# Performance work log

Hardware: AMD Instinct MI355X
Metric: run time of the kernel (lower is better)

The kernel has to match this reference:

```python
import jax, jax.numpy as jnp
import numpy as np

N_NODES = 50000      # nodes
N_EDGES = 800000     # directed edges (avg degree 16)
HIDDEN = 128
F_IN = 11            # QM9 num_node_features
NUM_CLASSES = 19     # QM9 num targets
NUM_GRAPHS = 2048


def _glorot(key, fan_in, fan_out):
    lim = np.sqrt(6.0 / (fan_in + fan_out)).astype(np.float32)
    return jax.random.uniform(key, (fan_in, fan_out), jnp.float32, -lim, lim)


def setup_inputs() -> dict:
    key = jax.random.key(0)
    ks = jax.random.split(key, 8)
    x = jax.random.normal(ks[0], (N_NODES, F_IN), jnp.float32)
    edge_index = jax.random.randint(ks[1], (2, N_EDGES), 0, N_NODES, dtype=jnp.int64)
    batch = jnp.sort(jax.random.randint(ks[2], (N_NODES,), 0, NUM_GRAPHS, dtype=jnp.int64))
    W1 = _glorot(ks[3], F_IN, HIDDEN); b1 = jnp.zeros((HIDDEN,), jnp.float32)
    W2 = _glorot(ks[4], HIDDEN, HIDDEN); b2 = jnp.zeros((HIDDEN,), jnp.float32)
    W3 = _glorot(ks[5], HIDDEN, HIDDEN); b3 = jnp.zeros((HIDDEN,), jnp.float32)
    Wl = _glorot(ks[6], HIDDEN, NUM_CLASSES); bl = jnp.zeros((NUM_CLASSES,), jnp.float32)
    return dict(x=x, edge_index=edge_index, batch=batch,
                W1=W1, b1=b1, W2=W2, b2=b2, W3=W3, b3=b3, Wl=Wl, bl=bl)


def gcn_conv(x, src, dst, W, b, n):
    """PyG GCNConv: x' = D^-1/2 (A + I) D^-1/2 (x W) + b, degrees include self-loops."""
    h = x @ W                                                      # [n, out]
    deg = jax.ops.segment_sum(jnp.ones_like(dst, h.dtype), dst, num_segments=n) + 1.0
    dinv = jax.lax.rsqrt(deg)                                      # [n]
    norm = dinv[src] * dinv[dst]                                   # [E]
    agg = jax.ops.segment_sum(h[src] * norm[:, None], dst, num_segments=n)
    agg = agg + h * (dinv * dinv)[:, None]                         # self-loop term
    return agg + b


def reference(x, edge_index, batch, W1, b1, W2, b2, W3, b3, Wl, bl):
    src, dst = edge_index[0], edge_index[1]
    h = jax.nn.relu(gcn_conv(x, src, dst, W1, b1, N_NODES))
    h = jax.nn.relu(gcn_conv(h, src, dst, W2, b2, N_NODES))
    h = gcn_conv(h, src, dst, W3, b3, N_NODES)
    # global_mean_pool over graph ids
    sums = jax.ops.segment_sum(h, batch, num_segments=NUM_GRAPHS)
    cnt = jax.ops.segment_sum(jnp.ones((N_NODES,), h.dtype), batch, num_segments=NUM_GRAPHS)
    pooled = sums / jnp.maximum(cnt, 1.0)[:, None]                 # [G, H]
    # dropout is identity in eval mode
    return pooled @ Wl + bl                                        # [G, NUM_CLASSES]
```

## Files before the change

### kernel.cpp

```cpp
#include <hip/hip_runtime.h>
#include <hip/hip_bf16.h>
#include <hip/hip_fp16.h>


#define HIDDEN 128
#define F_IN 11
#define NCLS 19
#define NBITS 9
#define NB 128
#define RNODES 512
#define EPB 8192
#define OUTL_CAP 10240

typedef _Float16 half8 __attribute__((ext_vector_type(8)));
typedef float floatx4 __attribute__((ext_vector_type(4)));


__global__ void scatter_kernel(const int* __restrict__ src, const int* __restrict__ dst,
                               int* __restrict__ bcur, unsigned int* __restrict__ bents,
                               int E, int cap) {
    __shared__ int hist[NB];
    __shared__ int binoff[NB];
    __shared__ int runrel[NB];
    __shared__ unsigned int ebuf[EPB];
    __shared__ unsigned short binOf[EPB];
    __shared__ int cw[2];
    int tid = threadIdx.x, lane = tid & 63, w = tid >> 6;
    int base = blockIdx.x * EPB;
    int cnt = min(EPB, E - base);
    for (int i = tid; i < NB; i += 256) hist[i] = 0;
    __syncthreads();
    unsigned int pk[32];
    int rk[32];
#pragma unroll
    for (int j = 0; j < 32; ++j) {
        int idx = tid + 256 * j;
        if (idx < cnt) {
            int e = base + idx;
            int s = src[e], d = dst[e];
            pk[j] = (unsigned int)s | ((unsigned int)d << 16);
            int bin = d >> NBITS;
            int r = atomicAdd(&hist[bin], 1);
            rk[j] = r | (bin << 16);
        } else rk[j] = -1;
    }
    __syncthreads();
    int v = 0, xv = 0;
    if (tid < NB) {
        v = hist[tid]; xv = v;
#pragma unroll
        for (int d = 1; d < 64; d <<= 1) {
            int t = __shfl_up(xv, d, 64);
            if (lane >= d) xv += t;
        }
        if (lane == 63) cw[w] = xv;
    }
    __syncthreads();
    if (tid < NB) {
        binoff[tid] = xv - v + ((w == 1) ? cw[0] : 0);
        runrel[tid] = v ? atomicAdd(&bcur[tid], v) : 0;
    }
    __syncthreads();
#pragma unroll
    for (int j = 0; j < 32; ++j) {
        if (rk[j] >= 0) {
            int bin = rk[j] >> 16, r = rk[j] & 0xFFFF;
            int pos = binoff[bin] + r;
            ebuf[pos] = pk[j];
            binOf[pos] = (unsigned short)bin;
        }
    }
    __syncthreads();
    for (int i = tid; i < cnt; i += 256) {
        int bin = binOf[i];
        int rel = runrel[bin] + (i - binoff[bin]);
        if (rel < cap)
            bents[bin * cap + rel] = ebuf[i];
    }
}

__global__ void build_kernel(const unsigned int* __restrict__ bents, const int* __restrict__ bcur,
                             const float* __restrict__ x, const int* __restrict__ batch,
                             int2* __restrict__ begend, unsigned short* __restrict__ csr16,
                             float* __restrict__ dinv, float* __restrict__ gcnt,
                             __half* __restrict__ x16h, int n, int cap, int rst) {
    __shared__ int counts[RNODES];
    __shared__ int lcur[RNODES];
    __shared__ unsigned short outl[OUTL_CAP];
    __shared__ int wsums[8];
    int tid = threadIdx.x;
    int lane = tid & 63, w = tid >> 6;
    int b = blockIdx.x;
    int base = b << NBITS;
    int nn = min(RNODES, n - base);
    int ebase = b * cap;
    int ecnt = min(bcur[b], cap);
    int st = b * rst;
    for (int i = tid; i < RNODES; i += 1024) counts[i] = 0;
    __syncthreads();
    for (int e = tid; e < ecnt; e += 1024)
        atomicAdd(&counts[(bents[ebase + e] >> 16) - base], 1);
    __syncthreads();
    int v = 0, xv = 0;
    if (tid < RNODES) {
        v = (tid < nn) ? counts[tid] + 1 : 0;
        xv = v;
#pragma unroll
        for (int d = 1; d < 64; d <<= 1) {
            int t = __shfl_up(xv, d, 64);
            if (lane >= d) xv += t;
        }
        if (lane == 63) wsums[w] = xv;
    }
    __syncthreads();
    if (tid < 64) {
        int s = (lane < 8) ? wsums[lane] : 0;
#pragma unroll
        for (int d = 1; d < 8; d <<= 1) {
            int t = __shfl_up(s, d, 64);
            if (lane >= d) s += t;
        }
        if (lane < 8) wsums[lane] = s;
    }
    __syncthreads();
    if (tid < nn) {
        int excl = xv - v + ((w > 0) ? wsums[w - 1] : 0);
        lcur[tid] = excl + 1;
        outl[excl] = (unsigned short)(base + tid);
        begend[base + tid] = make_int2(st + excl, st + excl + v);
        atomicAdd(&gcnt[batch[base + tid]], 1.0f);
    }
    __syncthreads();
    for (int e = tid; e < ecnt; e += 1024) {
        unsigned int pk = bents[ebase + e];
        int i = (int)(pk >> 16) - base;
        int r = atomicAdd(&lcur[i], 1);
        outl[r] = (unsigned short)(pk & 0xFFFFu);
    }
    __syncthreads();
    int total = ecnt + nn;
    for (int i = tid; i < total; i += 1024)
        csr16[st + i] = outl[i];
    for (int idx = tid; idx < nn * 16; idx += 1024) {
        int i = idx >> 4, j = idx & 15;
        float di = 1.0f / sqrtf((float)(counts[i] + 1));
        if (j == 0) dinv[base + i] = di;
        float xv2 = (j < F_IN) ? x[(long)(base + i) * F_IN + j] * di : 0.f;
        x16h[(long)(base + i) * 16 + j] = __float2half(xv2);
    }
}


__global__ void agg16_gemm_kernel(const __half* __restrict__ x16h, const int2* __restrict__ begend,
                                  const unsigned short* __restrict__ csr16,
                                  const float* __restrict__ dinv, const float* __restrict__ W1,
                                  const float* __restrict__ b1, __half* __restrict__ h1h, int n) {
    __shared__ float2 W1s[F_IN][64];
    __shared__ float2 bs[64];
    int tid = threadIdx.x;
    for (int i = tid; i < F_IN * 64; i += 256) {
        int k = i >> 6, j = i & 63;
        W1s[k][j] = make_float2(W1[k * HIDDEN + 2 * j], W1[k * HIDDEN + 2 * j + 1]);
    }
    if (tid < 64) bs[tid] = make_float2(b1[2 * tid], b1[2 * tid + 1]);
    __syncthreads();
    int node = (int)(((long)blockIdx.x * blockDim.x + threadIdx.x) >> 6);
    int lane = threadIdx.x & 63;
    if (node >= n) return;
    int grp = lane >> 4, f = lane & 15;
    int2 be = begend[node];
    int beg = be.x, end = be.y;
    float acc = 0.f;
    int eb = beg;
    for (; eb + 16 <= end; eb += 16) {
        int s[4]; __half v[4];
#pragma unroll
        for (int j = 0; j < 4; ++j) s[j] = csr16[eb + grp + 4 * j];
#pragma unroll
        for (int j = 0; j < 4; ++j) v[j] = x16h[(long)s[j] * 16 + f];
#pragma unroll
        for (int j = 0; j < 4; ++j) acc += __half2float(v[j]);
    }
    if (eb + 8 <= end) {
        int s0 = csr16[eb + grp], s1 = csr16[eb + grp + 4];
        acc += __half2float(x16h[(long)s0 * 16 + f]) + __half2float(x16h[(long)s1 * 16 + f]);
        eb += 8;
    }
    for (int e = eb + grp; e < end; e += 4)
        acc += __half2float(x16h[(long)csr16[e] * 16 + f]);
    acc += __shfl_down(acc, 32);
    acc += __shfl_down(acc, 16);
    float z = acc * dinv[node];
    float2 o = bs[lane];
#pragma unroll
    for (int k = 0; k < F_IN; ++k) {
        float zk = __shfl(z, k);
        float2 w = W1s[k][lane];
        o.x += zk * w.x;
        o.y += zk * w.y;
    }
    __half2 h = __floats2half2_rn(fmaxf(o.x, 0.f), fmaxf(o.y, 0.f));
    ((__half2*)h1h)[(long)node * 64 + lane] = h;
}


__global__ __launch_bounds__(256) void gemm_mfma_kernel(
        const __half* __restrict__ h1h, const float* __restrict__ W2,
        const float* __restrict__ dinv, __half* __restrict__ hsh, int n) {
    __shared__ _Float16 W2T[128 * 136];
    __shared__ _Float16 outs[64 * 136];
    int tid = threadIdx.x;
    for (int i = tid; i < 128 * 128; i += 256) {
        int k = i >> 7, nn = i & 127;
        W2T[nn * 136 + k] = (_Float16)W2[i];
    }
    int base = blockIdx.x * 64;
    int lane = tid & 63, wid = tid >> 6;
    int l15 = lane & 15, quad = lane >> 4;
    int arow = base + wid * 16 + l15;
    if (arow >= n) arow = n - 1;
    const _Float16* Aptr = (const _Float16*)h1h + (size_t)arow * 128;
    floatx4 acc[8];
#pragma unroll
    for (int t = 0; t < 8; ++t) acc[t] = (floatx4){0.f, 0.f, 0.f, 0.f};
    __syncthreads();
#pragma unroll
    for (int c = 0; c < 4; ++c) {
        half8 a = *(const half8*)(Aptr + c * 32 + quad * 8);
#pragma unroll
        for (int t = 0; t < 8; ++t) {
            half8 b = *(const half8*)(&W2T[(t * 16 + l15) * 136 + c * 32 + quad * 8]);
            acc[t] = __builtin_amdgcn_mfma_f32_16x16x32_f16(a, b, acc[t], 0, 0, 0);
        }
    }
    float dv[4];
#pragma unroll
    for (int r = 0; r < 4; ++r) {
        int nd = base + wid * 16 + quad * 4 + r;
        dv[r] = dinv[(nd < n) ? nd : 0];
    }
#pragma unroll
    for (int t = 0; t < 8; ++t)
#pragma unroll
        for (int r = 0; r < 4; ++r)
            outs[(wid * 16 + quad * 4 + r) * 136 + t * 16 + l15] = (_Float16)(acc[t][r] * dv[r]);
    __syncthreads();
    for (int i = tid; i < 64 * 16; i += 256) {
        int ln = i >> 4, qq = i & 15;
        long nd = base + ln;
        if (nd < n) {
            uint4 u = *(uint4*)&outs[ln * 136 + qq * 8];
            ((uint4*)hsh)[nd * 16 + qq] = u;
        }
    }
}


__global__ void agg128h_kernel(const __half* __restrict__ hsh, const int2* __restrict__ begend,
                               const unsigned short* __restrict__ csr16, const float* __restrict__ dinv,
                               const float* __restrict__ bias, __half* __restrict__ outh, int n) {
    int node = (int)(((long)blockIdx.x * blockDim.x + threadIdx.x) >> 6);
    int lane = threadIdx.x & 63;
    if (node >= n) return;
    int grp = lane >> 5, q = lane & 31;
    int2 be = begend[node];
    int beg = be.x, end = be.y;
    float4 acc = make_float4(0.f, 0.f, 0.f, 0.f);
    int eb = beg;
    for (; eb + 16 <= end; eb += 16) {
        int s[8]; uint2 u[8];
#pragma unroll
        for (int j = 0; j < 8; ++j) s[j] = csr16[eb + grp + 2 * j];
#pragma unroll
        for (int j = 0; j < 8; ++j) u[j] = ((const uint2*)hsh)[(long)s[j] * 32 + q];
#pragma unroll
        for (int j = 0; j < 8; ++j) {
            float2 lo = __half22float2(*(__half2*)&u[j].x);
            float2 hi = __half22float2(*(__half2*)&u[j].y);
            acc.x += lo.x; acc.y += lo.y; acc.z += hi.x; acc.w += hi.y;
        }
    }
    if (eb + 8 <= end) {
        int s[4]; uint2 u[4];
#pragma unroll
        for (int j = 0; j < 4; ++j) s[j] = csr16[eb + grp + 2 * j];
#pragma unroll
        for (int j = 0; j < 4; ++j) u[j] = ((const uint2*)hsh)[(long)s[j] * 32 + q];
#pragma unroll
        for (int j = 0; j < 4; ++j) {
            float2 lo = __half22float2(*(__half2*)&u[j].x);
            float2 hi = __half22float2(*(__half2*)&u[j].y);
            acc.x += lo.x; acc.y += lo.y; acc.z += hi.x; acc.w += hi.y;
        }
        eb += 8;
    }
    for (int e = eb + grp; e < end; e += 2) {
        uint2 u = ((const uint2*)hsh)[(long)csr16[e] * 32 + q];
        float2 lo = __half22float2(*(__half2*)&u.x);
        float2 hi = __half22float2(*(__half2*)&u.y);
        acc.x += lo.x; acc.y += lo.y; acc.z += hi.x; acc.w += hi.y;
    }
    acc.x += __shfl_down(acc.x, 32);
    acc.y += __shfl_down(acc.y, 32);
    acc.z += __shfl_down(acc.z, 32);
    acc.w += __shfl_down(acc.w, 32);
    if (grp == 0) {
        float di = dinv[node];
        float4 b = ((const float4*)bias)[q];
        __half2 h01 = __floats2half2_rn(fmaxf(acc.x * di + b.x, 0.f), fmaxf(acc.y * di + b.y, 0.f));
        __half2 h23 = __floats2half2_rn(fmaxf(acc.z * di + b.z, 0.f), fmaxf(acc.w * di + b.w, 0.f));
        uint2 u = make_uint2(*(unsigned int*)&h01, *(unsigned int*)&h23);
        ((uint2*)outh)[(long)node * 32 + q] = u;
    }
}


__global__ void w3l_kernel(const float* __restrict__ W3, const float* __restrict__ Wl,
                           const float* __restrict__ b3, float* __restrict__ W3l,
                           float* __restrict__ b3l) {
    __shared__ float Wls[HIDDEN * NCLS];
    int tid = threadIdx.x;
    for (int i = tid; i < HIDDEN * NCLS; i += 256) Wls[i] = Wl[i];
    __syncthreads();
    if (blockIdx.x < 10) {
        int o = blockIdx.x * 256 + tid;
        if (o < HIDDEN * NCLS) {
            int i = o / NCLS, j = o % NCLS;
            float acc = 0.f;
#pragma unroll 8
            for (int k = 0; k < HIDDEN; ++k) acc += W3[i * HIDDEN + k] * Wls[k * NCLS + j];
            W3l[o] = acc;
        }
    } else if (tid < NCLS) {
        float acc = 0.f;
#pragma unroll 8
        for (int k = 0; k < HIDDEN; ++k) acc += b3[k] * Wls[k * NCLS + tid];
        b3l[tid] = acc;
    }
}

__global__ void gemm_y32h_kernel(const __half* __restrict__ h2h, const float* __restrict__ W3l,
                                 const float* __restrict__ dinv, __half* __restrict__ ys, int n) {
    __shared__ float hs[12][HIDDEN];
    __shared__ float Ws[HIDDEN][20];
    int tid = threadIdx.x;
    long base = (long)blockIdx.x * 12;
    for (int i = tid; i < HIDDEN * NCLS; i += 256) Ws[i / NCLS][i % NCLS] = W3l[i];
    for (int idx = tid; idx < 12 * 32; idx += 256) {
        int node = idx >> 5, q = idx & 31;
        long gn = base + node;
        uint2 u = (gn < n) ? ((const uint2*)h2h)[gn * 32 + q] : make_uint2(0u, 0u);
        float2 lo = __half22float2(*(__half2*)&u.x);
        float2 hi = __half22float2(*(__half2*)&u.y);
        hs[node][q * 4] = lo.x; hs[node][q * 4 + 1] = lo.y;
        hs[node][q * 4 + 2] = hi.x; hs[node][q * 4 + 3] = hi.y;
    }
    __syncthreads();
    if (tid < 12 * NCLS) {
        int node = tid / NCLS, j = tid % NCLS;
        long gn = base + node;
        if (gn < n) {
            float acc = 0.f;
#pragma unroll 8
            for (int k = 0; k < HIDDEN; ++k) acc += hs[node][k] * Ws[k][j];
            ys[gn * 32 + j] = __float2half(acc * dinv[gn]);
        }
    }
    for (int idx = tid; idx < 12 * 13; idx += 256) {
        int node = idx / 13, j = 19 + idx % 13;
        long gn = base + node;
        if (gn < n) ys[gn * 32 + j] = __half(0.f);
    }
}

__global__ void agg24h_pool_kernel(const __half* __restrict__ ys, const int2* __restrict__ begend,
                                   const unsigned short* __restrict__ csr16, const float* __restrict__ dinv,
                                   const int* __restrict__ batch, float* __restrict__ pool, int n) {
    int node = (int)(((long)blockIdx.x * blockDim.x + threadIdx.x) >> 6);
    int lane = threadIdx.x & 63;
    if (node >= n) return;
    int grp = lane >> 4, f = lane & 15;
    int2 be = begend[node];
    int beg = be.x, end = be.y;
    float2 acc = {0.f, 0.f};
    int eb = beg;
    for (; eb + 32 <= end; eb += 32) {
        int s[8]; unsigned int u[8];
#pragma unroll
        for (int j = 0; j < 8; ++j) s[j] = csr16[eb + grp + 4 * j];
#pragma unroll
        for (int j = 0; j < 8; ++j) u[j] = ((const unsigned int*)ys)[(long)s[j] * 16 + f];
#pragma unroll
        for (int j = 0; j < 8; ++j) {
            float2 v = __half22float2(*(__half2*)&u[j]);
            acc.x += v.x; acc.y += v.y;
        }
    }
    if (eb + 16 <= end) {
        int s[4]; unsigned int u[4];
#pragma unroll
        for (int j = 0; j < 4; ++j) s[j] = csr16[eb + grp + 4 * j];
#pragma unroll
        for (int j = 0; j < 4; ++j) u[j] = ((const unsigned int*)ys)[(long)s[j] * 16 + f];
#pragma unroll
        for (int j = 0; j < 4; ++j) {
            float2 v = __half22float2(*(__half2*)&u[j]);
            acc.x += v.x; acc.y += v.y;
        }
        eb += 16;
    }
    for (int e = eb + grp; e < end; e += 4) {
        unsigned int u = ((const unsigned int*)ys)[(long)csr16[e] * 16 + f];
        float2 v = __half22float2(*(__half2*)&u);
        acc.x += v.x; acc.y += v.y;
    }
    acc.x += __shfl_down(acc.x, 32);
    acc.y += __shfl_down(acc.y, 32);
    acc.x += __shfl_down(acc.x, 16);
    acc.y += __shfl_down(acc.y, 16);
    if (lane < 16) {
        int g = batch[node];
        float sc = dinv[node];
        int c0 = 2 * f;
        if (c0 < NCLS) atomicAdd(&pool[(long)g * 24 + c0], acc.x * sc);
        if (c0 + 1 < NCLS) atomicAdd(&pool[(long)g * 24 + c0 + 1], acc.y * sc);
    }
}

__global__ void final_kernel(const float* __restrict__ pool, const float* __restrict__ cnt,
                             const float* __restrict__ b3l, const float* __restrict__ bl,
                             float* __restrict__ out, int G) {
    int i = blockIdx.x * blockDim.x + threadIdx.x;
    if (i >= G * NCLS) return;
    int g = i / NCLS, j = i % NCLS;
    float c = cnt[g];
    out[i] = (c > 0.f) ? pool[(long)g * 24 + j] / c + b3l[j] + bl[j] : bl[j];
}


static inline size_t align256(size_t x) { return (x + 255) & ~(size_t)255; }

extern "C" void kernel_launch(void* const* d_in, const int* in_sizes, int n_in,
                              void* d_out, int out_size, void* d_ws, size_t ws_size,
                              hipStream_t stream) {
    const float* x    = (const float*)d_in[0];
    const int*   ei   = (const int*)d_in[1];
    const int*   batch= (const int*)d_in[2];
    const float* W1   = (const float*)d_in[3];
    const float* b1   = (const float*)d_in[4];
    const float* W2   = (const float*)d_in[5];
    const float* b2   = (const float*)d_in[6];
    const float* W3   = (const float*)d_in[7];
    const float* b3   = (const float*)d_in[8];
    const float* Wl   = (const float*)d_in[9];
    const float* bl   = (const float*)d_in[10];
    float* out = (float*)d_out;

    const int N = in_sizes[0] / F_IN;
    const int E = in_sizes[1] / 2;
    const int G = out_size / NCLS;
    const int* src = ei;
    const int* dst = ei + E;
    const int nSB = (E + EPB - 1) / EPB;
    const int nBK = (N + RNODES - 1) / RNODES;
    int cap = (int)((long long)E * RNODES / N) + 1024;
    if (cap + RNODES > OUTL_CAP) cap = OUTL_CAP - RNODES;
    const int rst = cap + RNODES;

    char* p = (char*)d_ws;
    size_t off = 0;
    unsigned int*   bents  = (unsigned int*)(p + off);   off = align256(off + (size_t)NB * cap * 4);
    unsigned short* csr16  = (unsigned short*)(p + off); off = align256(off + (size_t)NB * rst * 2);
    int2*           begend = (int2*)(p + off);           off = align256(off + (size_t)N * 8);
    float*          dinv   = (float*)(p + off);          off = align256(off + (size_t)N * 4);
    __half*         x16h   = (__half*)(p + off);         off = align256(off + (size_t)N * 16 * 2);
    __half*         h1h    = (__half*)(p + off);         off = align256(off + (size_t)N * HIDDEN * 2);
    __half*         hsh    = (__half*)(p + off);         off = align256(off + (size_t)N * HIDDEN * 2);
    __half*         h2h    = (__half*)(p + off);         off = align256(off + (size_t)N * HIDDEN * 2);
    __half*         y32h   = (__half*)(p + off);         off = align256(off + (size_t)N * 32 * 2);
    float*          W3l    = (float*)(p + off);          off = align256(off + (size_t)HIDDEN * NCLS * 4);
    float*          b3l    = (float*)(p + off);          off = align256(off + (size_t)NCLS * 4);
    float*          pool   = (float*)(p + off);
    float*          gcnt   = pool + (size_t)G * 24;
    int*            bcur   = (int*)(pool + (size_t)G * 25);
    off = align256(off + (size_t)G * 25 * 4 + NB * 4);
    (void)ws_size; (void)n_in;

    hipMemsetAsync(pool, 0, (size_t)G * 25 * 4 + NB * 4, stream);

    scatter_kernel<<<nSB, 256, 0, stream>>>(src, dst, bcur, bents, E, cap);
    build_kernel<<<nBK, 1024, 0, stream>>>(bents, bcur, x, batch, begend, csr16,
                                           dinv, gcnt, x16h, N, cap, rst);
    w3l_kernel<<<11, 256, 0, stream>>>(W3, Wl, b3, W3l, b3l);

    const int aggBlocks = (N + 3) / 4;

    agg16_gemm_kernel<<<aggBlocks, 256, 0, stream>>>(x16h, begend, csr16, dinv, W1, b1, h1h, N);

    gemm_mfma_kernel<<<(N + 63) / 64, 256, 0, stream>>>(h1h, W2, dinv, hsh, N);
    agg128h_kernel<<<aggBlocks, 256, 0, stream>>>(hsh, begend, csr16, dinv, b2, h2h, N);

    gemm_y32h_kernel<<<(N + 11) / 12, 256, 0, stream>>>(h2h, W3l, dinv, y32h, N);
    agg24h_pool_kernel<<<aggBlocks, 256, 0, stream>>>(y32h, begend, csr16, dinv, batch, pool, N);
    final_kernel<<<(G * NCLS + 255) / 256, 256, 0, stream>>>(pool, gcnt, b3l, bl, out, G);
}
```

Before: 247.2 us.

## Shrink CSR bucket size, fold weight prep into scatter kernel, pretranspose W2

Halves the node-bucket width (256 nodes per bucket, 256 buckets) and edges per scatter block, so the build kernel runs with 512 threads and uses less shared memory. This gives more blocks and better occupancy in the CSR construction. The separate W3·Wl kernel is removed and its work, plus a one-time fp16 transpose of W2, runs in extra blocks of the scatter launch. The MFMA GEMM then copies the transposed W2 with vector loads instead of converting fp32 element by element in every block. The smaller bucket capacity margin raises overflow risk for skewed degree distributions.

Measured after the change: 231.0 us, median of 2. 1.07x faster.

```diff
diff --git a/kernel.cpp b/kernel.cpp
--- a/kernel.cpp
+++ b/kernel.cpp
@@ -6,11 +6,11 @@
 #define HIDDEN 128
 #define F_IN 11
 #define NCLS 19
-#define NBITS 9
-#define NB 128
-#define RNODES 512
-#define EPB 8192
-#define OUTL_CAP 10240
+#define NBITS 8
+#define NB 256
+#define RNODES 256
+#define EPB 4096
+#define OUTL_CAP 5376
 
 typedef _Float16 half8 __attribute__((ext_vector_type(8)));
 typedef float floatx4 __attribute__((ext_vector_type(4)));
@@ -18,22 +18,60 @@
 
 __global__ void scatter_kernel(const int* __restrict__ src, const int* __restrict__ dst,
                                int* __restrict__ bcur, unsigned int* __restrict__ bents,
-                               int E, int cap) {
+                               int E, int cap, int nSB,
+                               const float* __restrict__ W3, const float* __restrict__ Wl,
+                               const float* __restrict__ b3, float* __restrict__ W3l,
+                               float* __restrict__ b3l, const float* __restrict__ W2,
+                               __half* __restrict__ W2Th) {
     __shared__ int hist[NB];
     __shared__ int binoff[NB];
     __shared__ int runrel[NB];
     __shared__ unsigned int ebuf[EPB];
     __shared__ unsigned short binOf[EPB];
-    __shared__ int cw[2];
+    __shared__ int cw[4];
     int tid = threadIdx.x, lane = tid & 63, w = tid >> 6;
+
+    if (blockIdx.x >= nSB) {
+        int xb = blockIdx.x - nSB;
+        if (xb < 11) {
+            float* Wls = (float*)ebuf;
+            for (int i = tid; i < HIDDEN * NCLS; i += 256) Wls[i] = Wl[i];
+            __syncthreads();
+            if (xb < 10) {
+                int o = xb * 256 + tid;
+                if (o < HIDDEN * NCLS) {
+                    int i = o / NCLS, j = o % NCLS;
+                    float acc = 0.f;
+#pragma unroll 8
+                    for (int k = 0; k < HIDDEN; ++k) acc += W3[i * HIDDEN + k] * Wls[k * NCLS + j];
+                    W3l[o] = acc;
+                }
+            } else if (tid < NCLS) {
+                float acc = 0.f;
+#pragma unroll 8
+                for (int k = 0; k < HIDDEN; ++k) acc += b3[k] * Wls[k * NCLS + tid];
+                b3l[tid] = acc;
+            }
+        } else {
+            int base = (xb - 11) * 4096;
+#pragma unroll
+            for (int r = 0; r < 16; ++r) {
+                int idx = base + tid + 256 * r;
+                int k = idx >> 7, nn2 = idx & 127;
+                W2Th[nn2 * HIDDEN + k] = __float2half(W2[idx]);
+            }
+        }
+        return;
+    }
+
     int base = blockIdx.x * EPB;
     int cnt = min(EPB, E - base);
     for (int i = tid; i < NB; i += 256) hist[i] = 0;
     __syncthreads();
-    unsigned int pk[32];
-    int rk[32];
-#pragma unroll
-    for (int j = 0; j < 32; ++j) {
+    unsigned int pk[16];
+    int rk[16];
+#pragma unroll
+    for (int j = 0; j < 16; ++j) {
         int idx = tid + 256 * j;
         if (idx < cnt) {
             int e = base + idx;
@@ -45,24 +83,21 @@
         } else rk[j] = -1;
     }
     __syncthreads();
-    int v = 0, xv = 0;
-    if (tid < NB) {
-        v = hist[tid]; xv = v;
-#pragma unroll
-        for (int d = 1; d < 64; d <<= 1) {
-            int t = __shfl_up(xv, d, 64);
-            if (lane >= d) xv += t;
-        }
-        if (lane == 63) cw[w] = xv;
-    }
-    __syncthreads();
-    if (tid < NB) {
-        binoff[tid] = xv - v + ((w == 1) ? cw[0] : 0);
-        runrel[tid] = v ? atomicAdd(&bcur[tid], v) : 0;
-    }
-    __syncthreads();
-#pragma unroll
-    for (int j = 0; j < 32; ++j) {
+    int v = hist[tid], xv = v;
+#pragma unroll
+    for (int d = 1; d < 64; d <<= 1) {
+        int t = __shfl_up(xv, d, 64);
+        if (lane >= d) xv += t;
+    }
+    if (lane == 63) cw[w] = xv;
+    __syncthreads();
+    int waveoff = 0;
+    for (int wi = 0; wi < w; ++wi) waveoff += cw[wi];
+    binoff[tid] = waveoff + xv - v;
+    runrel[tid] = v ? atomicAdd(&bcur[tid], v) : 0;
+    __syncthreads();
+#pragma unroll
+    for (int j = 0; j < 16; ++j) {
         if (rk[j] >= 0) {
             int bin = rk[j] >> 16, r = rk[j] & 0xFFFF;
             int pos = binoff[bin] + r;
@@ -87,7 +122,7 @@
     __shared__ int counts[RNODES];
     __shared__ int lcur[RNODES];
     __shared__ unsigned short outl[OUTL_CAP];
-    __shared__ int wsums[8];
+    __shared__ int wsums[4];
     int tid = threadIdx.x;
     int lane = tid & 63, w = tid >> 6;
     int b = blockIdx.x;
@@ -96,9 +131,9 @@
     int ebase = b * cap;
     int ecnt = min(bcur[b], cap);
     int st = b * rst;
-    for (int i = tid; i < RNODES; i += 1024) counts[i] = 0;
-    __syncthreads();
-    for (int e = tid; e < ecnt; e += 1024)
+    for (int i = tid; i < RNODES; i += 512) counts[i] = 0;
+    __syncthreads();
+    for (int e = tid; e < ecnt; e += 512)
         atomicAdd(&counts[(bents[ebase + e] >> 16) - base], 1);
     __syncthreads();
     int v = 0, xv = 0;
@@ -113,25 +148,17 @@
         if (lane == 63) wsums[w] = xv;
     }
     __syncthreads();
-    if (tid < 64) {
-        int s = (lane < 8) ? wsums[lane] : 0;
-#pragma unroll
-        for (int d = 1; d < 8; d <<= 1) {
-            int t = __shfl_up(s, d, 64);
-            if (lane >= d) s += t;
-        }
-        if (lane < 8) wsums[lane] = s;
-    }
-    __syncthreads();
     if (tid < nn) {
-        int excl = xv - v + ((w > 0) ? wsums[w - 1] : 0);
+        int waveoff = 0;
+        for (int wi = 0; wi < w; ++wi) waveoff += wsums[wi];
+        int excl = waveoff + xv - v;
         lcur[tid] = excl + 1;
         outl[excl] = (unsigned short)(base + tid);
         begend[base + tid] = make_int2(st + excl, st + excl + v);
         atomicAdd(&gcnt[batch[base + tid]], 1.0f);
     }
     __syncthreads();
-    for (int e = tid; e < ecnt; e += 1024) {
+    for (int e = tid; e < ecnt; e += 512) {
         unsigned int pk = bents[ebase + e];
         int i = (int)(pk >> 16) - base;
         int r = atomicAdd(&lcur[i], 1);
@@ -139,9 +166,9 @@
     }
     __syncthreads();
     int total = ecnt + nn;
-    for (int i = tid; i < total; i += 1024)
+    for (int i = tid; i < total; i += 512)
         csr16[st + i] = outl[i];
-    for (int idx = tid; idx < nn * 16; idx += 1024) {
+    for (int idx = tid; idx < nn * 16; idx += 512) {
         int i = idx >> 4, j = idx & 15;
         float di = 1.0f / sqrtf((float)(counts[i] + 1));
         if (j == 0) dinv[base + i] = di;
@@ -205,14 +232,14 @@
 
 
 __global__ __launch_bounds__(256) void gemm_mfma_kernel(
-        const __half* __restrict__ h1h, const float* __restrict__ W2,
+        const __half* __restrict__ h1h, const __half* __restrict__ W2Th,
         const float* __restrict__ dinv, __half* __restrict__ hsh, int n) {
     __shared__ _Float16 W2T[128 * 136];
     __shared__ _Float16 outs[64 * 136];
     int tid = threadIdx.x;
-    for (int i = tid; i < 128 * 128; i += 256) {
-        int k = i >> 7, nn = i & 127;
-        W2T[nn * 136 + k] = (_Float16)W2[i];
+    for (int i = tid; i < 128 * 16; i += 256) {
+        int r = i >> 4, q = i & 15;
+        *(uint4*)&W2T[r * 136 + q * 8] = ((const uint4*)W2Th)[r * 16 + q];
     }
     int base = blockIdx.x * 64;
     int lane = tid & 63, wid = tid >> 6;
@@ -314,30 +341,6 @@
     }
 }
 
-
-__global__ void w3l_kernel(const float* __restrict__ W3, const float* __restrict__ Wl,
-                           const float* __restrict__ b3, float* __restrict__ W3l,
-                           float* __restrict__ b3l) {
-    __shared__ float Wls[HIDDEN * NCLS];
-    int tid = threadIdx.x;
-    for (int i = tid; i < HIDDEN * NCLS; i += 256) Wls[i] = Wl[i];
-    __syncthreads();
-    if (blockIdx.x < 10) {
-        int o = blockIdx.x * 256 + tid;
-        if (o < HIDDEN * NCLS) {
-            int i = o / NCLS, j = o % NCLS;
-            float acc = 0.f;
-#pragma unroll 8
-            for (int k = 0; k < HIDDEN; ++k) acc += W3[i * HIDDEN + k] * Wls[k * NCLS + j];
-            W3l[o] = acc;
-        }
-    } else if (tid < NCLS) {
-        float acc = 0.f;
-#pragma unroll 8
-        for (int k = 0; k < HIDDEN; ++k) acc += b3[k] * Wls[k * NCLS + tid];
-        b3l[tid] = acc;
-    }
-}
 
 __global__ void gemm_y32h_kernel(const __half* __restrict__ h2h, const float* __restrict__ W3l,
                                  const float* __restrict__ dinv, __half* __restrict__ ys, int n) {
@@ -463,7 +466,7 @@
     const int* dst = ei + E;
     const int nSB = (E + EPB - 1) / EPB;
     const int nBK = (N + RNODES - 1) / RNODES;
-    int cap = (int)((long long)E * RNODES / N) + 1024;
+    int cap = (int)((long long)E * RNODES / N) + 768;
     if (cap + RNODES > OUTL_CAP) cap = OUTL_CAP - RNODES;
     const int rst = cap + RNODES;
 
@@ -478,6 +481,7 @@
     __half*         hsh    = (__half*)(p + off);         off = align256(off + (size_t)N * HIDDEN * 2);
     __half*         h2h    = (__half*)(p + off);         off = align256(off + (size_t)N * HIDDEN * 2);
     __half*         y32h   = (__half*)(p + off);         off = align256(off + (size_t)N * 32 * 2);
+    __half*         W2Th   = (__half*)(p + off);         off = align256(off + (size_t)HIDDEN * HIDDEN * 2);
     float*          W3l    = (float*)(p + off);          off = align256(off + (size_t)HIDDEN * NCLS * 4);
     float*          b3l    = (float*)(p + off);          off = align256(off + (size_t)NCLS * 4);
     float*          pool   = (float*)(p + off);
@@ -488,16 +492,16 @@
 
     hipMemsetAsync(pool, 0, (size_t)G * 25 * 4 + NB * 4, stream);
 
-    scatter_kernel<<<nSB, 256, 0, stream>>>(src, dst, bcur, bents, E, cap);
-    build_kernel<<<nBK, 1024, 0, stream>>>(bents, bcur, x, batch, begend, csr16,
-                                           dinv, gcnt, x16h, N, cap, rst);
-    w3l_kernel<<<11, 256, 0, stream>>>(W3, Wl, b3, W3l, b3l);
+    scatter_kernel<<<nSB + 15, 256, 0, stream>>>(src, dst, bcur, bents, E, cap, nSB,
+                                                 W3, Wl, b3, W3l, b3l, W2, W2Th);
+    build_kernel<<<nBK, 512, 0, stream>>>(bents, bcur, x, batch, begend, csr16,
+                                          dinv, gcnt, x16h, N, cap, rst);
 
     const int aggBlocks = (N + 3) / 4;
 
     agg16_gemm_kernel<<<aggBlocks, 256, 0, stream>>>(x16h, begend, csr16, dinv, W1, b1, h1h, N);
 
-    gemm_mfma_kernel<<<(N + 63) / 64, 256, 0, stream>>>(h1h, W2, dinv, hsh, N);
+    gemm_mfma_kernel<<<(N + 63) / 64, 256, 0, stream>>>(h1h, W2Th, dinv, hsh, N);
     agg128h_kernel<<<aggBlocks, 256, 0, stream>>>(hsh, begend, csr16, dinv, b2, h2h, N);
 
     gemm_y32h_kernel<<<(N + 11) / 12, 256, 0, stream>>>(h2h, W3l, dinv, y32h, N);
```
